# Kernel tuning notes

Hardware: AMD Instinct MI355X
Metric: run time of the kernel (lower is better)

Reference implementation:

```python
import jax, jax.numpy as jnp
import numpy as np

B, T, C, H = 8, 2048, 768, 12
D = C // H

def setup_inputs() -> dict:
    key = jax.random.key(0)
    ks = jax.random.split(key, 5)
    s = 0.02
    return {
        "x": jax.random.normal(ks[0], (B, T, C), dtype=jnp.float32),
        "w_attn": jax.random.normal(ks[1], (C, 3 * C), dtype=jnp.float32) * s,
        "b_attn": jnp.zeros((3 * C,), dtype=jnp.float32),
        "w_proj": jax.random.normal(ks[2], (C, C), dtype=jnp.float32) * s,
        "b_proj": jnp.zeros((C,), dtype=jnp.float32),
    }

def reference(x, w_attn, b_attn, w_proj, b_proj):
    Bx, Tx, Cx = x.shape
    qkv = x @ w_attn + b_attn                       # [B,T,3C]
    q, k, v = jnp.split(qkv, 3, axis=-1)
    # [B,H,T,D]
    q = q.reshape(Bx, Tx, H, D).transpose(0, 2, 1, 3)
    k = k.reshape(Bx, Tx, H, D).transpose(0, 2, 1, 3)
    v = v.reshape(Bx, Tx, H, D).transpose(0, 2, 1, 3)
    scale = 1.0 / jnp.sqrt(jnp.float32(D))
    att = jnp.einsum('bhqd,bhkd->bhqk', q, k) * scale
    causal = jnp.tril(jnp.ones((Tx, Tx), dtype=bool))
    att = jnp.where(causal[None, None], att, -jnp.inf)
    att = jax.nn.softmax(att, axis=-1)
    y = jnp.einsum('bhqk,bhkd->bhqd', att, v)
    y = y.transpose(0, 2, 1, 3).reshape(Bx, Tx, Cx)
    y = y @ w_proj + b_proj
    return y, k, v
```

## Files before the change

### kernel.cpp

```cpp
#include <hip/hip_runtime.h>
#include <hip/hip_bf16.h>
#include <stdint.h>

#define Bz 8
#define Tz 2048
#define Cz 768
#define Hz 12
#define Dz 64
#define Mz (Bz*Tz)
#define N3 (3*Cz)
#define YSZ ((size_t)Mz*Cz)

#define SCL 0.18033688011112042f
#define KVB 64
#define QBLK 128

typedef __bf16 bf16;
typedef __attribute__((ext_vector_type(8))) bf16 bf16x8;
typedef __attribute__((ext_vector_type(4))) bf16 bf16x4;
typedef __attribute__((ext_vector_type(4))) float f32x4;

#define MFMA(A_,B_,C_) __builtin_amdgcn_mfma_f32_16x16x32_bf16(A_,B_,C_,0,0,0)

__device__ __forceinline__ void gll16(const void* g, void* l) {
  __builtin_amdgcn_global_load_lds(
      (const __attribute__((address_space(1))) void*)g,
      (__attribute__((address_space(3))) void*)l, 16, 0, 0);
}

__global__ __launch_bounds__(256) void prep_x(const float* __restrict__ x,
                                              bf16* __restrict__ xb) {
  int i = blockIdx.x*blockDim.x + threadIdx.x;
  int stride = gridDim.x*blockDim.x;
  const float4* x4 = (const float4*)x;
  int n4 = (int)(YSZ/4);
  for (int j = i; j < n4; j += stride) {
    float4 f = x4[j];
    bf16x4 o = { (bf16)f.x, (bf16)f.y, (bf16)f.z, (bf16)f.w };
    *(bf16x4*)(xb + 4*(size_t)j) = o;
  }
}

__global__ __launch_bounds__(256) void transpose_conv(const float* __restrict__ src,
                                                      bf16* __restrict__ dst,
                                                      int R, int Ncol) {
  __shared__ float tile[32][33];
  int bx = blockIdx.x, by = blockIdx.y;
  int tx = threadIdx.x & 31, ty = threadIdx.x >> 5;
  #pragma unroll
  for (int i = 0; i < 4; ++i)
    tile[ty + 8*i][tx] = src[(size_t)(by*32 + ty + 8*i)*Ncol + bx*32 + tx];
  __syncthreads();
  #pragma unroll
  for (int i = 0; i < 4; ++i)
    dst[(size_t)(bx*32 + ty + 8*i)*R + by*32 + tx] = (bf16)tile[tx][ty + 8*i];
}

template<int EPI>
__global__ __launch_bounds__(256) void gemm128(
    const bf16* __restrict__ A, const bf16* __restrict__ Bt,
    int Kdim, int Mtiles, int Ntiles,
    const float* __restrict__ bias,
    bf16* __restrict__ qws, bf16* __restrict__ kws, bf16* __restrict__ vtb,
    float* __restrict__ kout, float* __restrict__ vout,
    float* __restrict__ yout)
{
  __shared__ alignas(16) bf16 sA[2][128*64];
  __shared__ alignas(16) bf16 sB[2][128*64];
  int nwg = Mtiles*Ntiles;
  int bid = blockIdx.x;
  int cpx = nwg >> 3;
  int swz = (bid & 7)*cpx + (bid >> 3);
  int ntile = swz % Ntiles, mtile = swz / Ntiles;
  int tid = threadIdx.x, w = tid >> 6, l = tid & 63;
  int wr = w >> 1, wc = w & 1;
  const int rowBase = mtile*128, colBase = ntile*128;

  f32x4 acc[4][4] = {};

  int rbase = tid >> 3;
  int ch    = tid & 7;
  int swk   = (ch ^ (rbase & 7)) << 3;
  const bf16* gA = A + (size_t)(rowBase + rbase)*Kdim + swk;
  const bf16* gB = Bt + (size_t)(colBase + rbase)*Kdim + swk;

  int lr = l & 15, lg = l >> 4;
  int nK = Kdim >> 6;

  {
    char* lA = (char*)sA[0] + w*1024;
    char* lB = (char*)sB[0] + w*1024;
    #pragma unroll
    for (int p = 0; p < 4; ++p) {
      gll16(gA + (size_t)(p*32)*Kdim, lA + p*4096);
      gll16(gB + (size_t)(p*32)*Kdim, lB + p*4096);
    }
    gA += 64; gB += 64;
  }
  int buf = 0;
  for (int t = 0; t < nK; ++t) {
    if (t + 1 < nK) {
      char* lA = (char*)sA[buf ^ 1] + w*1024;
      char* lB = (char*)sB[buf ^ 1] + w*1024;
      #pragma unroll
      for (int p = 0; p < 4; ++p) {
        gll16(gA + (size_t)(p*32)*Kdim, lA + p*4096);
        gll16(gB + (size_t)(p*32)*Kdim, lB + p*4096);
      }
      gA += 64; gB += 64;
      asm volatile("s_waitcnt vmcnt(8)" ::: "memory");
    } else {
      asm volatile("s_waitcnt vmcnt(0)" ::: "memory");
    }
    __builtin_amdgcn_s_barrier();
    __builtin_amdgcn_sched_barrier(0);
    const char* cA = (const char*)sA[buf];
    const char* cB = (const char*)sB[buf];
    __builtin_amdgcn_s_setprio(1);
    #pragma unroll
    for (int kk = 0; kk < 2; ++kk) {
      bf16x8 af[4], bfr[4];
      int cc = ((kk*4 + lg) ^ (lr & 7)) << 4;
      #pragma unroll
      for (int m = 0; m < 4; ++m)
        af[m] = *(const bf16x8*)(cA + (wr*64 + m*16 + lr)*128 + cc);
      #pragma unroll
      for (int n = 0; n < 4; ++n)
        bfr[n] = *(const bf16x8*)(cB + (wc*64 + n*16 + lr)*128 + cc);
      #pragma unroll
      for (int m = 0; m < 4; ++m)
        #pragma unroll
        for (int n = 0; n < 4; ++n)
          acc[m][n] = MFMA(af[m], bfr[n], acc[m][n]);
    }
    __builtin_amdgcn_s_setprio(0);
    asm volatile("s_waitcnt lgkmcnt(0)" ::: "memory");
    __builtin_amdgcn_s_barrier();
    __builtin_amdgcn_sched_barrier(0);
    buf ^= 1;
  }

  #pragma unroll
  for (int m = 0; m < 4; ++m) {
    #pragma unroll
    for (int n = 0; n < 4; ++n) {
      int gcol = colBase + wc*64 + n*16 + lr;
      float bv = bias[gcol];
      int grow0 = rowBase + wr*64 + m*16 + lg*4;
      if (EPI == 1) {
        #pragma unroll
        for (int r = 0; r < 4; ++r)
          yout[(size_t)(grow0 + r)*Cz + gcol] = acc[m][n][r] + bv;
      } else {
        int which = gcol / Cz;
        int within = gcol - which*Cz;
        int h = within >> 6, d = within & 63;
        int bidx = grow0 >> 11;
        int t0 = grow0 & 2047;
        size_t bhTD = ((size_t)bidx*Hz + h);
        if (which == 0) {
          bf16* qp = qws + (bhTD*Tz + t0)*Dz + d;
          #pragma unroll
          for (int r = 0; r < 4; ++r)
            qp[(size_t)r*Dz] = (bf16)((acc[m][n][r] + bv) * SCL);
        } else if (which == 1) {
          float* kp = kout + (bhTD*Tz + t0)*Dz + d;
          bf16*  kp2 = kws + (bhTD*Tz + t0)*Dz + d;
          #pragma unroll
          for (int r = 0; r < 4; ++r) {
            float v = acc[m][n][r] + bv;
            kp[(size_t)r*Dz] = v;
            kp2[(size_t)r*Dz] = (bf16)v;
          }
        } else {
          float* vp = vout + (bhTD*Tz + t0)*Dz + d;
          bf16x4 pk;
          #pragma unroll
          for (int r = 0; r < 4; ++r) {
            float v = acc[m][n][r] + bv;
            vp[(size_t)r*Dz] = v;
            pk[r] = (bf16)v;
          }
          int ts = (t0 & ~31) | (((t0 >> 2) & 3) << 3) | (((t0 >> 4) & 1) << 2) | (t0 & 3);
          *(bf16x4*)(vtb + (bhTD*Dz + d)*Tz + ts) = pk;
        }
      }
    }
  }
}

__device__ __forceinline__ void attn_tile(
    int kv0, int qminw, int qmaxw, int q_l, int lr, int lg,
    const char* cK, const char* cV,
    const bf16x8& qf0, const bf16x8& qf1, const bf16x8& ones,
    f32x4 (&o)[4], f32x4& lsum, float& mrun)
{
  const f32x4 zf = {0.f, 0.f, 0.f, 0.f};
  f32x4 s[4];
  __builtin_amdgcn_s_setprio(1);
  #pragma unroll
  for (int n = 0; n < 4; ++n) {
    int kvb = kv0 + n*16;
    if (kvb <= qmaxw) {
      int row = n*16 + lr;
      int c0 = lg ^ (lr & 7);
      bf16x8 kf0 = *(const bf16x8*)(cK + row*128 + (c0 << 4));
      bf16x8 kf1 = *(const bf16x8*)(cK + row*128 + ((c0 ^ 4) << 4));
      f32x4 t = MFMA(kf0, qf0, zf);
      s[n] = MFMA(kf1, qf1, t);
    } else {
      s[n][0] = -1e30f; s[n][1] = -1e30f; s[n][2] = -1e30f; s[n][3] = -1e30f;
    }
  }
  __builtin_amdgcn_s_setprio(0);
  #pragma unroll
  for (int n = 0; n < 4; ++n) {
    int kvb = kv0 + n*16;
    if (kvb <= qmaxw && kvb + 15 > qminw) {
      #pragma unroll
      for (int r = 0; r < 4; ++r)
        s[n][r] = (kvb + 4*lg + r <= q_l) ? s[n][r] : -1e30f;
    }
  }
  f32x4 a0;
  #pragma unroll
  for (int r = 0; r < 4; ++r)
    a0[r] = fmaxf(fmaxf(s[0][r], s[1][r]), fmaxf(s[2][r], s[3][r]));
  float mx = fmaxf(fmaxf(a0[0], a0[1]), fmaxf(a0[2], a0[3]));
  mx = fmaxf(mx, __shfl_xor(mx, 16));
  mx = fmaxf(mx, __shfl_xor(mx, 32));

  bool skip = __all(mx <= mrun + 8.0f);
  if (!skip) {
    float mnew = fmaxf(mrun, mx);
    float corr = exp2f(mrun - mnew);
    mrun = mnew;
    float c0_ = __shfl(corr, 4*lg + 0);
    float c1_ = __shfl(corr, 4*lg + 1);
    float c2_ = __shfl(corr, 4*lg + 2);
    float c3_ = __shfl(corr, 4*lg + 3);
    #pragma unroll
    for (int nd = 0; nd < 4; ++nd) {
      o[nd][0] *= c0_; o[nd][1] *= c1_; o[nd][2] *= c2_; o[nd][3] *= c3_;
    }
    lsum[0] *= c0_; lsum[1] *= c1_; lsum[2] *= c2_; lsum[3] *= c3_;
  }
  #pragma unroll
  for (int n = 0; n < 4; ++n) {
    #pragma unroll
    for (int r = 0; r < 4; ++r)
      s[n][r] = exp2f(s[n][r] - mrun);
  }
  __builtin_amdgcn_s_setprio(1);
  #pragma unroll
  for (int kk = 0; kk < 2; ++kk) {
    if (kv0 + kk*32 <= qmaxw) {
      bf16x8 pf;
      pf[0] = (bf16)s[2*kk][0];   pf[1] = (bf16)s[2*kk][1];
      pf[2] = (bf16)s[2*kk][2];   pf[3] = (bf16)s[2*kk][3];
      pf[4] = (bf16)s[2*kk+1][0]; pf[5] = (bf16)s[2*kk+1][1];
      pf[6] = (bf16)s[2*kk+1][2]; pf[7] = (bf16)s[2*kk+1][3];
      lsum = MFMA(pf, ones, lsum);
      int cb = (kk*4 + lg) ^ (lr & 7);
      #pragma unroll
      for (int nd = 0; nd < 4; ++nd) {
        bf16x8 vf = *(const bf16x8*)(cV + (nd*16 + lr)*128 + (cb << 4));
        o[nd] = MFMA(pf, vf, o[nd]);
      }
    }
  }
  __builtin_amdgcn_s_setprio(0);
}

__global__ __launch_bounds__(512, 6) void attn128(
    const bf16* __restrict__ qws, const bf16* __restrict__ kb,
    const bf16* __restrict__ vtb, bf16* __restrict__ yatt)
{
  __shared__ alignas(16) char sK[2][8192];
  __shared__ alignas(16) char sV[2][8192];
  int bid = blockIdx.x;
  int qb = (Tz/QBLK) - 1 - bid/(Bz*Hz);
  int bh = bid % (Bz*Hz);
  int b = bh / Hz, h = bh - b*Hz;
  int tid = threadIdx.x, w = tid >> 6, l = tid & 63;
  int lr = l & 15, lg = l >> 4;
  const int q0 = qb*QBLK;
  const int qminw = q0 + w*16;
  const int qmaxw = qminw + 15;
  const int q_l = qminw + lr;

  const bf16* qbase = qws + ((size_t)bh*Tz + qminw + lr)*Dz + lg*8;
  bf16x8 qf0 = *(const bf16x8*)qbase;
  bf16x8 qf1 = *(const bf16x8*)(qbase + 32);

  bf16 onev = (bf16)1.0f;
  bf16x8 ones = { onev, onev, onev, onev, onev, onev, onev, onev };

  f32x4 o[4] = {};
  f32x4 lsum = {0.f, 0.f, 0.f, 0.f};
  float mrun = -1e30f;

  int srow = tid >> 3;
  int ssw  = ((tid & 7) ^ (srow & 7)) << 3;
  const bf16* kp = kb  + (size_t)bh*Tz*Dz + (size_t)srow*Dz + ssw;
  const bf16* vp = vtb + (size_t)bh*Dz*Tz + (size_t)srow*Tz + ssw;
  char* dK0 = sK[0] + w*1024;  char* dV0 = sV[0] + w*1024;
  char* dK1 = sK[1] + w*1024;  char* dV1 = sV[1] + w*1024;

  int nT = 2*qb + 2;
  gll16(kp, dK0); gll16(vp, dV0); kp += (size_t)KVB*Dz; vp += KVB;

  for (int kt = 0; kt < nT; kt += 2) {
    gll16(kp, dK1); gll16(vp, dV1); kp += (size_t)KVB*Dz; vp += KVB;
    asm volatile("s_waitcnt vmcnt(2)" ::: "memory");
    __builtin_amdgcn_s_barrier();
    __builtin_amdgcn_sched_barrier(0);
    attn_tile(kt*KVB, qminw, qmaxw, q_l, lr, lg, sK[0], sV[0],
              qf0, qf1, ones, o, lsum, mrun);
    asm volatile("s_waitcnt lgkmcnt(0)" ::: "memory");
    __builtin_amdgcn_s_barrier();
    __builtin_amdgcn_sched_barrier(0);
    if (kt + 2 < nT) {
      gll16(kp, dK0); gll16(vp, dV0); kp += (size_t)KVB*Dz; vp += KVB;
      asm volatile("s_waitcnt vmcnt(2)" ::: "memory");
    } else {
      asm volatile("s_waitcnt vmcnt(0)" ::: "memory");
    }
    __builtin_amdgcn_s_barrier();
    __builtin_amdgcn_sched_barrier(0);
    attn_tile((kt + 1)*KVB, qminw, qmaxw, q_l, lr, lg, sK[1], sV[1],
              qf0, qf1, ones, o, lsum, mrun);
    if (kt + 2 < nT) {
      asm volatile("s_waitcnt lgkmcnt(0)" ::: "memory");
      __builtin_amdgcn_s_barrier();
      __builtin_amdgcn_sched_barrier(0);
    }
  }

  f32x4 inv;
  #pragma unroll
  for (int r = 0; r < 4; ++r) inv[r] = 1.0f / lsum[r];
  #pragma unroll
  for (int nd = 0; nd < 4; ++nd) {
    int d = nd*16 + lr;
    int t0 = q0 + w*16 + lg*4;
    bf16* yp = yatt + ((size_t)(b*Tz + t0))*Cz + h*Dz + d;
    yp[0*Cz]   = (bf16)(o[nd][0] * inv[0]);
    yp[1*Cz]   = (bf16)(o[nd][1] * inv[1]);
    yp[2*Cz]   = (bf16)(o[nd][2] * inv[2]);
    yp[3*Cz]   = (bf16)(o[nd][3] * inv[3]);
  }
}

extern "C" void kernel_launch(void* const* d_in, const int* in_sizes, int n_in,
                              void* d_out, int out_size, void* d_ws, size_t ws_size,
                              hipStream_t stream) {
  const float* x      = (const float*)d_in[0];
  const float* w_attn = (const float*)d_in[1];
  const float* b_attn = (const float*)d_in[2];
  const float* w_proj = (const float*)d_in[3];
  const float* b_proj = (const float*)d_in[4];

  float* y    = (float*)d_out;
  float* kout = y + YSZ;
  float* vout = y + 2*YSZ;

  char* ws = (char*)d_ws;
  bf16* xb   = (bf16*)ws;
  bf16* qws  = (bf16*)(ws + 25165824);
  bf16* kb   = (bf16*)(ws + 50331648);
  bf16* vtb  = (bf16*)(ws + 75497472);
  bf16* wtA  = (bf16*)(ws + 100663296);
  bf16* wtP  = (bf16*)(ws + 104202240);
  bf16* yatt = xb;

  prep_x<<<2048, 256, 0, stream>>>(x, xb);
  transpose_conv<<<dim3(N3/32, Cz/32), 256, 0, stream>>>(w_attn, wtA, Cz, N3);
  transpose_conv<<<dim3(Cz/32, Cz/32), 256, 0, stream>>>(w_proj, wtP, Cz, Cz);

  gemm128<0><<<dim3((Mz/128)*(N3/128)), 256, 0, stream>>>(
      xb, wtA, Cz, Mz/128, N3/128, b_attn, qws, kb, vtb, kout, vout, nullptr);

  attn128<<<dim3((Tz/QBLK)*(Bz*Hz)), 512, 0, stream>>>(qws, kb, vtb, yatt);

  gemm128<1><<<dim3((Mz/128)*(Cz/128)), 256, 0, stream>>>(
      yatt, wtP, Cz, Mz/128, Cz/128, b_proj, nullptr, nullptr, nullptr,
      nullptr, nullptr, y);
}
```

Baseline: 266.5 us.

## Widen attention KV tile to 128 and restructure double-buffered load loop

Doubles the KV block processed per attention tile from 64 to 128 keys. This halves the number of barrier and softmax-rescale steps per query block and gives longer MFMA runs between synchronisations. The main loop becomes a single-tile ping-pong over two LDS buffers instead of an unrolled pair, and the V tile gets a new 16-wide swizzle for the wider rows. In exchange, LDS use doubles to 64 KB per block, register pressure rises from 8 score vectors, and occupancy drops (launch bounds go from 6 to 4). Causal waste on diagonal tiles also grows.

```diff
diff --git a/kernel.cpp b/kernel.cpp
--- a/kernel.cpp
+++ b/kernel.cpp
@@ -12,7 +12,7 @@
 #define YSZ ((size_t)Mz*Cz)
 
 #define SCL 0.18033688011112042f
-#define KVB 64
+#define KVB 128
 #define QBLK 128
 
 typedef __bf16 bf16;
@@ -196,10 +196,10 @@
     f32x4 (&o)[4], f32x4& lsum, float& mrun)
 {
   const f32x4 zf = {0.f, 0.f, 0.f, 0.f};
-  f32x4 s[4];
+  f32x4 s[8];
   __builtin_amdgcn_s_setprio(1);
   #pragma unroll
-  for (int n = 0; n < 4; ++n) {
+  for (int n = 0; n < 8; ++n) {
     int kvb = kv0 + n*16;
     if (kvb <= qmaxw) {
       int row = n*16 + lr;
@@ -214,7 +214,7 @@
   }
   __builtin_amdgcn_s_setprio(0);
   #pragma unroll
-  for (int n = 0; n < 4; ++n) {
+  for (int n = 0; n < 8; ++n) {
     int kvb = kv0 + n*16;
     if (kvb <= qmaxw && kvb + 15 > qminw) {
       #pragma unroll
@@ -222,11 +222,14 @@
         s[n][r] = (kvb + 4*lg + r <= q_l) ? s[n][r] : -1e30f;
     }
   }
-  f32x4 a0;
-  #pragma unroll
-  for (int r = 0; r < 4; ++r)
+  f32x4 a0, a1;
+  #pragma unroll
+  for (int r = 0; r < 4; ++r) {
     a0[r] = fmaxf(fmaxf(s[0][r], s[1][r]), fmaxf(s[2][r], s[3][r]));
-  float mx = fmaxf(fmaxf(a0[0], a0[1]), fmaxf(a0[2], a0[3]));
+    a1[r] = fmaxf(fmaxf(s[4][r], s[5][r]), fmaxf(s[6][r], s[7][r]));
+  }
+  float mx = fmaxf(fmaxf(fmaxf(a0[0], a0[1]), fmaxf(a0[2], a0[3])),
+                   fmaxf(fmaxf(a1[0], a1[1]), fmaxf(a1[2], a1[3])));
   mx = fmaxf(mx, __shfl_xor(mx, 16));
   mx = fmaxf(mx, __shfl_xor(mx, 32));
 
@@ -246,14 +249,14 @@
     lsum[0] *= c0_; lsum[1] *= c1_; lsum[2] *= c2_; lsum[3] *= c3_;
   }
   #pragma unroll
-  for (int n = 0; n < 4; ++n) {
+  for (int n = 0; n < 8; ++n) {
     #pragma unroll
     for (int r = 0; r < 4; ++r)
       s[n][r] = exp2f(s[n][r] - mrun);
   }
   __builtin_amdgcn_s_setprio(1);
   #pragma unroll
-  for (int kk = 0; kk < 2; ++kk) {
+  for (int kk = 0; kk < 4; ++kk) {
     if (kv0 + kk*32 <= qmaxw) {
       bf16x8 pf;
       pf[0] = (bf16)s[2*kk][0];   pf[1] = (bf16)s[2*kk][1];
@@ -261,10 +264,10 @@
       pf[4] = (bf16)s[2*kk+1][0]; pf[5] = (bf16)s[2*kk+1][1];
       pf[6] = (bf16)s[2*kk+1][2]; pf[7] = (bf16)s[2*kk+1][3];
       lsum = MFMA(pf, ones, lsum);
-      int cb = (kk*4 + lg) ^ (lr & 7);
+      int cb = (kk*4 + lg) ^ lr;
       #pragma unroll
       for (int nd = 0; nd < 4; ++nd) {
-        bf16x8 vf = *(const bf16x8*)(cV + (nd*16 + lr)*128 + (cb << 4));
+        bf16x8 vf = *(const bf16x8*)(cV + (nd*16 + lr)*256 + (cb << 4));
         o[nd] = MFMA(pf, vf, o[nd]);
       }
     }
@@ -272,12 +275,12 @@
   __builtin_amdgcn_s_setprio(0);
 }
 
-__global__ __launch_bounds__(512, 6) void attn128(
+__global__ __launch_bounds__(512, 4) void attn128(
     const bf16* __restrict__ qws, const bf16* __restrict__ kb,
     const bf16* __restrict__ vtb, bf16* __restrict__ yatt)
 {
-  __shared__ alignas(16) char sK[2][8192];
-  __shared__ alignas(16) char sV[2][8192];
+  __shared__ alignas(16) char sK[2][16384];
+  __shared__ alignas(16) char sV[2][16384];
   int bid = blockIdx.x;
   int qb = (Tz/QBLK) - 1 - bid/(Bz*Hz);
   int bh = bid % (Bz*Hz);
@@ -300,41 +303,42 @@
   f32x4 lsum = {0.f, 0.f, 0.f, 0.f};
   float mrun = -1e30f;
 
-  int srow = tid >> 3;
-  int ssw  = ((tid & 7) ^ (srow & 7)) << 3;
-  const bf16* kp = kb  + (size_t)bh*Tz*Dz + (size_t)srow*Dz + ssw;
-  const bf16* vp = vtb + (size_t)bh*Dz*Tz + (size_t)srow*Tz + ssw;
+  int krow = tid >> 3;
+  int ksw  = ((tid & 7) ^ (krow & 7)) << 3;
+  int vrow = tid >> 4;
+  int vsw  = ((tid & 15) ^ (vrow & 15)) << 3;
+  const bf16* kp = kb  + (size_t)bh*Tz*Dz + (size_t)krow*Dz + ksw;
+  const bf16* vp = vtb + (size_t)bh*Dz*Tz + (size_t)vrow*Tz + vsw;
   char* dK0 = sK[0] + w*1024;  char* dV0 = sV[0] + w*1024;
   char* dK1 = sK[1] + w*1024;  char* dV1 = sV[1] + w*1024;
 
-  int nT = 2*qb + 2;
-  gll16(kp, dK0); gll16(vp, dV0); kp += (size_t)KVB*Dz; vp += KVB;
-
-  for (int kt = 0; kt < nT; kt += 2) {
-    gll16(kp, dK1); gll16(vp, dV1); kp += (size_t)KVB*Dz; vp += KVB;
-    asm volatile("s_waitcnt vmcnt(2)" ::: "memory");
+  int nT = qb + 1;
+  gll16(kp, dK0); gll16(kp + (size_t)64*Dz, dK0 + 8192);
+  gll16(vp, dV0); gll16(vp + (size_t)32*Tz, dV0 + 8192);
+  kp += (size_t)KVB*Dz; vp += KVB;
+
+  int buf = 0;
+  for (int kt = 0; kt < nT; ++kt) {
+    if (kt + 1 < nT) {
+      char* dK = buf ? dK0 : dK1;
+      char* dV = buf ? dV0 : dV1;
+      gll16(kp, dK); gll16(kp + (size_t)64*Dz, dK + 8192);
+      gll16(vp, dV); gll16(vp + (size_t)32*Tz, dV + 8192);
+      kp += (size_t)KVB*Dz; vp += KVB;
+      asm volatile("s_waitcnt vmcnt(4)" ::: "memory");
+    } else {
+      asm volatile("s_waitcnt vmcnt(0)" ::: "memory");
+    }
     __builtin_amdgcn_s_barrier();
     __builtin_amdgcn_sched_barrier(0);
-    attn_tile(kt*KVB, qminw, qmaxw, q_l, lr, lg, sK[0], sV[0],
+    attn_tile(kt*KVB, qminw, qmaxw, q_l, lr, lg, sK[buf], sV[buf],
               qf0, qf1, ones, o, lsum, mrun);
-    asm volatile("s_waitcnt lgkmcnt(0)" ::: "memory");
-    __builtin_amdgcn_s_barrier();
-    __builtin_amdgcn_sched_barrier(0);
-    if (kt + 2 < nT) {
-      gll16(kp, dK0); gll16(vp, dV0); kp += (size_t)KVB*Dz; vp += KVB;
-      asm volatile("s_waitcnt vmcnt(2)" ::: "memory");
-    } else {
-      asm volatile("s_waitcnt vmcnt(0)" ::: "memory");
-    }
-    __builtin_amdgcn_s_barrier();
-    __builtin_amdgcn_sched_barrier(0);
-    attn_tile((kt + 1)*KVB, qminw, qmaxw, q_l, lr, lg, sK[1], sV[1],
-              qf0, qf1, ones, o, lsum, mrun);
-    if (kt + 2 < nT) {
+    if (kt + 1 < nT) {
       asm volatile("s_waitcnt lgkmcnt(0)" ::: "memory");
       __builtin_amdgcn_s_barrier();
       __builtin_amdgcn_sched_barrier(0);
     }
+    buf ^= 1;
   }
 
   f32x4 inv;
```

After: 266.6 us. Within noise of the previous version (+0.0%).

## Software-pipeline QK of next tile with softmax/PV of previous tile

Applied to the files above, without the earlier changes.

Splits the attention tile into a QK-score step and a softmax+PV step, then interleaves them so the QK MFMAs for tile k+1 are issued alongside softmax and PV for tile k. A third V shared buffer lets V stay live one iteration longer. Loads are now waited fully with vmcnt(0) before each barrier rather than overlapping two in flight. Launch bounds drop from 6 to 4 waves per EU, which gives more registers for the extra score tiles but lowers occupancy.

```diff
diff --git a/kernel.cpp b/kernel.cpp
--- a/kernel.cpp
+++ b/kernel.cpp
@@ -189,14 +189,11 @@
   }
 }
 
-__device__ __forceinline__ void attn_tile(
+__device__ __forceinline__ void qk_tile(
     int kv0, int qminw, int qmaxw, int q_l, int lr, int lg,
-    const char* cK, const char* cV,
-    const bf16x8& qf0, const bf16x8& qf1, const bf16x8& ones,
-    f32x4 (&o)[4], f32x4& lsum, float& mrun)
+    const char* cK, const bf16x8& qf0, const bf16x8& qf1, f32x4 (&s)[4])
 {
   const f32x4 zf = {0.f, 0.f, 0.f, 0.f};
-  f32x4 s[4];
   __builtin_amdgcn_s_setprio(1);
   #pragma unroll
   for (int n = 0; n < 4; ++n) {
@@ -222,6 +219,13 @@
         s[n][r] = (kvb + 4*lg + r <= q_l) ? s[n][r] : -1e30f;
     }
   }
+}
+
+__device__ __forceinline__ void sm_pv(
+    int kv0, int qmaxw, int lr, int lg,
+    const char* cV, const bf16x8& ones,
+    f32x4 (&s)[4], f32x4 (&o)[4], f32x4& lsum, float& mrun)
+{
   f32x4 a0;
   #pragma unroll
   for (int r = 0; r < 4; ++r)
@@ -272,12 +276,12 @@
   __builtin_amdgcn_s_setprio(0);
 }
 
-__global__ __launch_bounds__(512, 6) void attn128(
+__global__ __launch_bounds__(512, 4) void attn128(
     const bf16* __restrict__ qws, const bf16* __restrict__ kb,
     const bf16* __restrict__ vtb, bf16* __restrict__ yatt)
 {
   __shared__ alignas(16) char sK[2][8192];
-  __shared__ alignas(16) char sV[2][8192];
+  __shared__ alignas(16) char sV[3][8192];
   int bid = blockIdx.x;
   int qb = (Tz/QBLK) - 1 - bid/(Bz*Hz);
   int bh = bid % (Bz*Hz);
@@ -299,43 +303,44 @@
   f32x4 o[4] = {};
   f32x4 lsum = {0.f, 0.f, 0.f, 0.f};
   float mrun = -1e30f;
+  f32x4 sA_[4], sB_[4];
 
   int srow = tid >> 3;
   int ssw  = ((tid & 7) ^ (srow & 7)) << 3;
   const bf16* kp = kb  + (size_t)bh*Tz*Dz + (size_t)srow*Dz + ssw;
   const bf16* vp = vtb + (size_t)bh*Dz*Tz + (size_t)srow*Tz + ssw;
-  char* dK0 = sK[0] + w*1024;  char* dV0 = sV[0] + w*1024;
-  char* dK1 = sK[1] + w*1024;  char* dV1 = sV[1] + w*1024;
+
+  char* kCur  = sK[0]; char* kNext = sK[1];
+  char* vPrev = sV[2]; char* vCur  = sV[0]; char* vNext = sV[1];
 
   int nT = 2*qb + 2;
-  gll16(kp, dK0); gll16(vp, dV0); kp += (size_t)KVB*Dz; vp += KVB;
+  gll16(kp, kCur + w*1024); gll16(vp, vCur + w*1024);
+  kp += (size_t)KVB*Dz; vp += KVB;
 
   for (int kt = 0; kt < nT; kt += 2) {
-    gll16(kp, dK1); gll16(vp, dV1); kp += (size_t)KVB*Dz; vp += KVB;
-    asm volatile("s_waitcnt vmcnt(2)" ::: "memory");
+    asm volatile("s_waitcnt vmcnt(0)" ::: "memory");
     __builtin_amdgcn_s_barrier();
     __builtin_amdgcn_sched_barrier(0);
-    attn_tile(kt*KVB, qminw, qmaxw, q_l, lr, lg, sK[0], sV[0],
-              qf0, qf1, ones, o, lsum, mrun);
-    asm volatile("s_waitcnt lgkmcnt(0)" ::: "memory");
+    gll16(kp, kNext + w*1024); gll16(vp, vNext + w*1024);
+    kp += (size_t)KVB*Dz; vp += KVB;
+    qk_tile(kt*KVB, qminw, qmaxw, q_l, lr, lg, kCur, qf0, qf1, sA_);
+    if (kt > 0)
+      sm_pv((kt - 1)*KVB, qmaxw, lr, lg, vPrev, ones, sB_, o, lsum, mrun);
+    { char* t1 = kCur; kCur = kNext; kNext = t1; }
+    { char* t2 = vPrev; vPrev = vCur; vCur = vNext; vNext = t2; }
+    asm volatile("s_waitcnt vmcnt(0)" ::: "memory");
     __builtin_amdgcn_s_barrier();
     __builtin_amdgcn_sched_barrier(0);
     if (kt + 2 < nT) {
-      gll16(kp, dK0); gll16(vp, dV0); kp += (size_t)KVB*Dz; vp += KVB;
-      asm volatile("s_waitcnt vmcnt(2)" ::: "memory");
-    } else {
-      asm volatile("s_waitcnt vmcnt(0)" ::: "memory");
-    }
-    __builtin_amdgcn_s_barrier();
-    __builtin_amdgcn_sched_barrier(0);
-    attn_tile((kt + 1)*KVB, qminw, qmaxw, q_l, lr, lg, sK[1], sV[1],
-              qf0, qf1, ones, o, lsum, mrun);
-    if (kt + 2 < nT) {
-      asm volatile("s_waitcnt lgkmcnt(0)" ::: "memory");
-      __builtin_amdgcn_s_barrier();
-      __builtin_amdgcn_sched_barrier(0);
-    }
-  }
+      gll16(kp, kNext + w*1024); gll16(vp, vNext + w*1024);
+      kp += (size_t)KVB*Dz; vp += KVB;
+    }
+    qk_tile((kt + 1)*KVB, qminw, qmaxw, q_l, lr, lg, kCur, qf0, qf1, sB_);
+    sm_pv(kt*KVB, qmaxw, lr, lg, vPrev, ones, sA_, o, lsum, mrun);
+    { char* t1 = kCur; kCur = kNext; kNext = t1; }
+    { char* t2 = vPrev; vPrev = vCur; vCur = vNext; vNext = t2; }
+  }
+  sm_pv((nT - 1)*KVB, qmaxw, lr, lg, vPrev, ones, sB_, o, lsum, mrun);
 
   f32x4 inv;
   #pragma unroll
```

Result: no change. 264.0 us (-0.9%).
